# Kernel tuning notes

Measured on AMD Instinct MI355X. Metric: run time of the kernel, lower is better.

Reference implementation:

```python
import jax, jax.numpy as jnp
import numpy as np

B, LQ, LM, D, H = 2, 2048, 2048, 1024, 16
DH = D // H  # 64

def setup_inputs() -> dict:
    key = jax.random.key(0)
    ks = jax.random.split(key, 11)
    s = 0.02
    return {
        "query": jax.random.normal(ks[0], (B, LQ, D), jnp.float32),
        "memory": jax.random.normal(ks[1], (B, LM, D), jnp.float32),
        "memory_bias": jax.random.normal(ks[2], (B, LM), jnp.float32),
        "Wq": jax.random.normal(ks[3], (D, D), jnp.float32) * s,
        "bq": jnp.zeros((D,), jnp.float32),
        "Wk": jax.random.normal(ks[4], (D, D), jnp.float32) * s,
        "bk": jnp.zeros((D,), jnp.float32),
        "Wv": jax.random.normal(ks[5], (D, D), jnp.float32) * s,
        "bv": jnp.zeros((D,), jnp.float32),
        "Wo": jax.random.normal(ks[6], (D, D), jnp.float32) * s,
        "bo": jnp.zeros((D,), jnp.float32),
    }

def reference(query, memory, memory_bias, Wq, bq, Wk, bk, Wv, bv, Wo, bo):
    # QKV projections, split into heads: [B, L, H, DH]
    q = (query @ Wq + bq).reshape(B, LQ, H, DH)
    k = (memory @ Wk + bk).reshape(B, LM, H, DH)
    v = (memory @ Wv + bv).reshape(B, LM, H, DH)
    q = q * (DH ** -0.5)
    # logits: [B, H, Lq, Lk] (matches torch.einsum('btnh,bfnh->bnft', k, q))
    logits = jnp.einsum("bfnh,btnh->bnft", q, k)
    logits = logits + memory_bias[:, None, None, :]  # bias [B, Lm] -> [B,1,1,Lk]
    weights = jax.nn.softmax(logits, axis=-1)
    # dropout omitted (eval / rate 0 for correctness baseline)
    attn = jnp.einsum("bnft,btnh->bfnh", weights, v).reshape(B, LQ, D)
    return attn @ Wo + bo  # [B, Lq, output_depth]
```

## Files before the change

kernel.cpp:

```cpp
#include <hip/hip_runtime.h>
#include <hip/hip_bf16.h>
#include <math.h>


typedef __bf16 bf16;
typedef __bf16 bf16x4 __attribute__((ext_vector_type(4)));
typedef __bf16 bf16x8 __attribute__((ext_vector_type(8)));
typedef float f32x4 __attribute__((ext_vector_type(4)));

#define MFMA16(a, b, c) __builtin_amdgcn_mfma_f32_16x16x32_bf16((a), (b), (c), 0, 0, 0)

__device__ inline float exp2_hw(float x) {
    float r; asm("v_exp_f32 %0, %1" : "=v"(r) : "v"(x)); return r;
}

__device__ inline void gload_lds16(const bf16* g, bf16* l) {
    __builtin_amdgcn_global_load_lds(
        (const __attribute__((address_space(1))) void*)g,
        (__attribute__((address_space(3))) void*)l, 16, 0, 0);
}

__global__ __launch_bounds__(256) void prep_kernel(
    const float* __restrict__ query, const float* __restrict__ memory,
    const float* __restrict__ mbias,
    const float* __restrict__ W0, const float* __restrict__ W1,
    const float* __restrict__ W2, const float* __restrict__ W3,
    bf16* __restrict__ Yq, bf16* __restrict__ Ym, float* __restrict__ sbias,
    bf16* __restrict__ T0, bf16* __restrict__ T1,
    bf16* __restrict__ T2, bf16* __restrict__ T3)
{
    __shared__ float Ls[64][65];
    const int t = threadIdx.x;

    if (blockIdx.z == 0) {
        const float* X = blockIdx.y ? memory : query;
        bf16* Y = blockIdx.y ? Ym : Yq;
        const size_t i = ((size_t)blockIdx.x * 256 + t) * 8;
        float4 f0 = *(const float4*)&X[i];
        float4 f1 = *(const float4*)&X[i + 4];
        bf16x8 h;
        h[0] = (bf16)f0.x; h[1] = (bf16)f0.y; h[2] = (bf16)f0.z; h[3] = (bf16)f0.w;
        h[4] = (bf16)f1.x; h[5] = (bf16)f1.y; h[6] = (bf16)f1.z; h[7] = (bf16)f1.w;
        *(bf16x8*)&Y[i] = h;
        return;
    }
    const int x = blockIdx.x;
    if (x == 1024) {
        const int i = blockIdx.y * 2048 + t * 8;
        #pragma unroll
        for (int j = 0; j < 8; ++j) sbias[i + j] = mbias[i + j] * 1.44269504f;
        return;
    }
    if (x > 1024 || blockIdx.y) return;

    const int wsel = x >> 8, sub = x & 255;
    const float* W; bf16* T;
    switch (wsel) {
        case 0:  W = W0; T = T0; break;
        case 1:  W = W1; T = T1; break;
        case 2:  W = W2; T = T2; break;
        default: W = W3; T = T3; break;
    }
    const int n0 = (sub & 15) * 64, k0 = (sub >> 4) * 64;
    const int g = t >> 4, c = (t & 15) * 4;
    #pragma unroll
    for (int p = 0; p < 4; ++p) {
        const int row = p * 16 + g;
        float4 f = *(const float4*)&W[(size_t)(k0 + row) * 1024 + n0 + c];
        Ls[row][c + 0] = f.x; Ls[row][c + 1] = f.y;
        Ls[row][c + 2] = f.z; Ls[row][c + 3] = f.w;
    }
    __syncthreads();
    #pragma unroll
    for (int p = 0; p < 4; ++p) {
        const int n = p * 16 + g;
        bf16x4 h;
        h[0] = (bf16)Ls[c + 0][n]; h[1] = (bf16)Ls[c + 1][n];
        h[2] = (bf16)Ls[c + 2][n]; h[3] = (bf16)Ls[c + 3][n];
        *(bf16x4*)&T[(size_t)(n0 + n) * 1024 + k0 + c] = h;
    }
}

template <typename TO>
__global__ __launch_bounds__(256) void gemm_kernel(
    const bf16* __restrict__ A, const bf16* __restrict__ WT,
    const float* __restrict__ bias, TO* __restrict__ out,
    float alpha, int mode)
{
    __shared__ __align__(16) bf16 As[2][128 * 64];
    __shared__ __align__(16) bf16 Bs[2][64 * 64];

    const int fid = blockIdx.x + (blockIdx.y << 4);
    const int swz = (fid & 7) * 64 + (fid >> 3);
    const int n0 = (swz & 15) * 64;
    const int m0 = (swz >> 4) * 128;

    const int tid = threadIdx.x;
    const int w = tid >> 6, lane = tid & 63;
    const int lr = lane & 15, lg = lane >> 4;
    const int wm = (w >> 1) * 64, wn = (w & 1) * 32;

    const int arow0 = w * 32 + (lane >> 3);
    const int brow0 = w * 16 + (lane >> 3);
    const int sch = lane & 7;

    f32x4 acc[4][2] = {};

    auto stageG = [&](int kt, int bi) {
        #pragma unroll
        for (int p = 0; p < 4; ++p) {
            const int row = arow0 + p * 8;
            const int xc = ((sch ^ (row & 7)) << 3);
            gload_lds16(&A[(size_t)(m0 + row) * 1024 + kt + xc],
                        &As[bi][row * 64 + sch * 8]);
        }
        #pragma unroll
        for (int p = 0; p < 2; ++p) {
            const int row = brow0 + p * 8;
            const int xc = ((sch ^ (row & 7)) << 3);
            gload_lds16(&WT[(size_t)(n0 + row) * 1024 + kt + xc],
                        &Bs[bi][row * 64 + sch * 8]);
        }
    };

    stageG(0, 0);
    __syncthreads();

    int cur = 0;
    #pragma unroll 1
    for (int t = 0; t < 16; ++t) {
        if (t < 15) stageG((t + 1) * 64, cur ^ 1);

        #pragma unroll
        for (int ks = 0; ks < 2; ++ks) {
            const int c = (((ks * 4 + lg) ^ (lr & 7)) << 3);
            bf16x8 af[4], bfv[2];
            #pragma unroll
            for (int mt = 0; mt < 4; ++mt)
                af[mt] = *(const bf16x8*)&As[cur][(wm + mt * 16 + lr) * 64 + c];
            #pragma unroll
            for (int nt = 0; nt < 2; ++nt)
                bfv[nt] = *(const bf16x8*)&Bs[cur][(wn + nt * 16 + lr) * 64 + c];
            #pragma unroll
            for (int nt = 0; nt < 2; ++nt)
                #pragma unroll
                for (int mt = 0; mt < 4; ++mt)
                    acc[mt][nt] = MFMA16(af[mt], bfv[nt], acc[mt][nt]);
        }
        __syncthreads();
        cur ^= 1;
    }

    #pragma unroll
    for (int nt = 0; nt < 2; ++nt) {
        const int n = n0 + wn + nt * 16 + lr;
        const float bv = bias[n];
        #pragma unroll
        for (int mt = 0; mt < 4; ++mt) {
            #pragma unroll
            for (int i = 0; i < 4; ++i) {
                const int m = m0 + wm + mt * 16 + lg * 4 + i;
                const float v = (acc[mt][nt][i] + bv) * alpha;
                if (mode == 0) {
                    out[(size_t)m * 1024 + n] = (TO)v;
                } else {
                    const int b = m >> 11, t2 = m & 2047;
                    out[((size_t)(b << 10) + n) * 2048 + t2] = (TO)v;
                }
            }
        }
    }
}

__global__ __launch_bounds__(256) void gemm_kv_kernel(
    const bf16* __restrict__ A, const bf16* __restrict__ WTk,
    const bf16* __restrict__ WTv, const float* __restrict__ bk,
    const float* __restrict__ bv, bf16* __restrict__ Kout,
    bf16* __restrict__ Vtout)
{
    __shared__ __align__(16) bf16 As[2][128 * 64];
    __shared__ __align__(16) bf16 Bk[2][64 * 64];
    __shared__ __align__(16) bf16 Bv[2][64 * 64];

    const int fid = blockIdx.x + (blockIdx.y << 4);
    const int swz = (fid & 7) * 64 + (fid >> 3);
    const int n0 = (swz & 15) * 64;
    const int m0 = (swz >> 4) * 128;

    const int tid = threadIdx.x;
    const int w = tid >> 6, lane = tid & 63;
    const int lr = lane & 15, lg = lane >> 4;
    const int wm = (w >> 1) * 64, wn = (w & 1) * 32;

    const int arow0 = w * 32 + (lane >> 3);
    const int brow0 = w * 16 + (lane >> 3);
    const int sch = lane & 7;

    f32x4 accK[4][2] = {}, accV[4][2] = {};

    auto stageG = [&](int kt, int bi) {
        #pragma unroll
        for (int p = 0; p < 4; ++p) {
            const int row = arow0 + p * 8;
            const int xc = ((sch ^ (row & 7)) << 3);
            gload_lds16(&A[(size_t)(m0 + row) * 1024 + kt + xc],
                        &As[bi][row * 64 + sch * 8]);
        }
        #pragma unroll
        for (int p = 0; p < 2; ++p) {
            const int row = brow0 + p * 8;
            const int xc = ((sch ^ (row & 7)) << 3);
            gload_lds16(&WTk[(size_t)(n0 + row) * 1024 + kt + xc],
                        &Bk[bi][row * 64 + sch * 8]);
            gload_lds16(&WTv[(size_t)(n0 + row) * 1024 + kt + xc],
                        &Bv[bi][row * 64 + sch * 8]);
        }
    };

    stageG(0, 0);
    __syncthreads();

    int cur = 0;
    #pragma unroll 1
    for (int t = 0; t < 16; ++t) {
        if (t < 15) stageG((t + 1) * 64, cur ^ 1);

        #pragma unroll
        for (int ks = 0; ks < 2; ++ks) {
            const int c = (((ks * 4 + lg) ^ (lr & 7)) << 3);
            bf16x8 af[4], bkf[2], bvf[2];
            #pragma unroll
            for (int mt = 0; mt < 4; ++mt)
                af[mt] = *(const bf16x8*)&As[cur][(wm + mt * 16 + lr) * 64 + c];
            #pragma unroll
            for (int nt = 0; nt < 2; ++nt) {
                bkf[nt] = *(const bf16x8*)&Bk[cur][(wn + nt * 16 + lr) * 64 + c];
                bvf[nt] = *(const bf16x8*)&Bv[cur][(wn + nt * 16 + lr) * 64 + c];
            }
            #pragma unroll
            for (int nt = 0; nt < 2; ++nt)
                #pragma unroll
                for (int mt = 0; mt < 4; ++mt) {
                    accK[mt][nt] = MFMA16(af[mt], bkf[nt], accK[mt][nt]);
                    accV[mt][nt] = MFMA16(af[mt], bvf[nt], accV[mt][nt]);
                }
        }
        __syncthreads();
        cur ^= 1;
    }

    #pragma unroll
    for (int nt = 0; nt < 2; ++nt) {
        const int n = n0 + wn + nt * 16 + lr;
        const float bkv = bk[n], bvv = bv[n];
        #pragma unroll
        for (int mt = 0; mt < 4; ++mt) {
            #pragma unroll
            for (int i = 0; i < 4; ++i) {
                const int m = m0 + wm + mt * 16 + lg * 4 + i;
                Kout[(size_t)m * 1024 + n] = (bf16)(accK[mt][nt][i] + bkv);
                const int b = m >> 11, t2 = m & 2047;
                Vtout[((size_t)(b << 10) + n) * 2048 + t2] = (bf16)(accV[mt][nt][i] + bvv);
            }
        }
    }
}

__global__ __launch_bounds__(512) void attn_kernel(
    const bf16* __restrict__ Q, const bf16* __restrict__ K,
    const bf16* __restrict__ Vt, const float* __restrict__ sbias,
    bf16* __restrict__ Oout)
{
    __shared__ __align__(16) bf16 Kbuf[4][4096];
    __shared__ __align__(16) bf16 Vbuf[4][4096];

    const int tid = threadIdx.x;
    const int w = tid >> 6, lane = tid & 63;
    const int lr = lane & 15, lg = lane >> 4;

    const int fid = blockIdx.x + (blockIdx.y << 3) + (blockIdx.z << 7);
    const int swz = (fid & 7) * 32 + (fid >> 3);
    const int qt = swz & 7, head = (swz >> 3) & 15, b = swz >> 7;
    const int qrow = qt * 256 + w * 32;

    bf16x8 qf[2][2];
    #pragma unroll
    for (int g = 0; g < 2; ++g) {
        const size_t qo = (size_t)(b * 2048 + qrow + g * 16 + lr) * 1024 + head * 64;
        qf[g][0] = *(const bf16x8*)&Q[qo + lg * 8];
        qf[g][1] = *(const bf16x8*)&Q[qo + 32 + lg * 8];
    }

    const bf16* Kb = K + (size_t)b * 2048 * 1024 + head * 64;
    const bf16* Vb = Vt + ((size_t)b * 1024 + head * 64) * 2048;
    const float* biasb = sbias + b * 2048;

    float m_run[2] = {-INFINITY, -INFINITY};
    f32x4 of[2][4] = {};
    f32x4 ofl[2] = {};

    bf16x8 ones8;
    #pragma unroll
    for (int j = 0; j < 8; ++j) ones8[j] = (bf16)1.0f;

    const int R = tid >> 3, cc = tid & 7;
    const int cs = cc ^ (R & 7);
    const int piR = ((R & 16) << 1) | ((R & 12) << 1) | ((R & 32) >> 3) | (R & 3);
    auto stage = [&](int t, int slot) {
        gload_lds16(Kb + (size_t)(t * 64 + piR) * 1024 + cs * 8,
                    &Kbuf[slot][tid * 8]);
        gload_lds16(Vb + (size_t)R * 2048 + t * 64 + cs * 8,
                    &Vbuf[slot][tid * 8]);
    };

    stage(0, 0);
    stage(1, 1);

    f32x4 b4[4];
    b4[0] = *(const f32x4*)&biasb[8 * lg];
    b4[1] = *(const f32x4*)&biasb[32 + 8 * lg];
    b4[2] = *(const f32x4*)&biasb[4 + 8 * lg];
    b4[3] = *(const f32x4*)&biasb[36 + 8 * lg];

    #pragma unroll 1
    for (int it = 0; it < 32; ++it) {
        const int slot = it & 3;
        const int tn = (it < 30) ? it + 2 : 31;
        stage(tn, (it + 2) & 3);
        asm volatile("s_waitcnt vmcnt(4)" ::: "memory");
        __builtin_amdgcn_s_barrier();
        __builtin_amdgcn_sched_barrier(0);

        const int bt = ((it < 31) ? it + 1 : 31) * 64;
        f32x4 b4n[4];
        b4n[0] = *(const f32x4*)&biasb[bt + 8 * lg];
        b4n[1] = *(const f32x4*)&biasb[bt + 32 + 8 * lg];
        b4n[2] = *(const f32x4*)&biasb[bt + 4 + 8 * lg];
        b4n[3] = *(const f32x4*)&biasb[bt + 36 + 8 * lg];

        f32x4 s[2][4];
        #pragma unroll
        for (int g = 0; g < 2; ++g)
            #pragma unroll
            for (int nt = 0; nt < 4; ++nt) s[g][nt] = b4[nt];
        #pragma unroll
        for (int ks = 0; ks < 2; ++ks) {
            const int cw = (((ks * 4 + lg) ^ (lr & 7)) << 3);
            bf16x8 kf[4];
            #pragma unroll
            for (int nt = 0; nt < 4; ++nt)
                kf[nt] = *(const bf16x8*)&Kbuf[slot][(nt * 16 + lr) * 64 + cw];
            __builtin_amdgcn_s_setprio(1);
            #pragma unroll
            for (int nt = 0; nt < 4; ++nt) {
                s[0][nt] = MFMA16(kf[nt], qf[0][ks], s[0][nt]);
                s[1][nt] = MFMA16(kf[nt], qf[1][ks], s[1][nt]);
            }
            __builtin_amdgcn_s_setprio(0);
        }

        bf16x8 vf[2][4];
        #pragma unroll
        for (int ks = 0; ks < 2; ++ks) {
            const int cw = (((ks * 4 + lg) ^ (lr & 7)) << 3);
            #pragma unroll
            for (int dt = 0; dt < 4; ++dt)
                vf[ks][dt] = *(const bf16x8*)&Vbuf[slot][(dt * 16 + lr) * 64 + cw];
        }

        float rml[2];
        #pragma unroll
        for (int g = 0; g < 2; ++g) {
            float m0 = fmaxf(fmaxf(s[g][0][0], s[g][0][1]), fmaxf(s[g][0][2], s[g][0][3]));
            float m1 = fmaxf(fmaxf(s[g][1][0], s[g][1][1]), fmaxf(s[g][1][2], s[g][1][3]));
            float m2 = fmaxf(fmaxf(s[g][2][0], s[g][2][1]), fmaxf(s[g][2][2], s[g][2][3]));
            float m3 = fmaxf(fmaxf(s[g][3][0], s[g][3][1]), fmaxf(s[g][3][2], s[g][3][3]));
            rml[g] = fmaxf(fmaxf(m0, m1), fmaxf(m2, m3));
        }
        const bool need = (rml[0] > m_run[0] + 8.f) || (rml[1] > m_run[1] + 8.f);

        if (__any(need)) {
            #pragma unroll
            for (int g = 0; g < 2; ++g) {
                float mx = fmaxf(rml[g], __shfl_xor(rml[g], 16, 64));
                mx = fmaxf(mx, __shfl_xor(mx, 32, 64));
                const float mnew = fmaxf(m_run[g], mx);
                const float al = exp2_hw(m_run[g] - mnew);
                m_run[g] = mnew;
                ofl[g] *= al;
                #pragma unroll
                for (int dt = 0; dt < 4; ++dt) of[g][dt] *= al;
            }
        }

        bf16x8 pb[2][2];
        #pragma unroll
        for (int g = 0; g < 2; ++g)
            #pragma unroll
            for (int i = 0; i < 4; ++i) {
                pb[g][0][i]     = (bf16)exp2_hw(s[g][0][i] - m_run[g]);
                pb[g][1][i]     = (bf16)exp2_hw(s[g][1][i] - m_run[g]);
                pb[g][0][4 + i] = (bf16)exp2_hw(s[g][2][i] - m_run[g]);
                pb[g][1][4 + i] = (bf16)exp2_hw(s[g][3][i] - m_run[g]);
            }

        __builtin_amdgcn_s_setprio(1);
        #pragma unroll
        for (int ks = 0; ks < 2; ++ks) {
            #pragma unroll
            for (int g = 0; g < 2; ++g) {
                #pragma unroll
                for (int dt = 0; dt < 4; ++dt)
                    of[g][dt] = MFMA16(vf[ks][dt], pb[g][ks], of[g][dt]);
                ofl[g] = MFMA16(ones8, pb[g][ks], ofl[g]);
            }
        }
        __builtin_amdgcn_s_setprio(0);

        #pragma unroll
        for (int nt = 0; nt < 4; ++nt) b4[nt] = b4n[nt];
    }

    #pragma unroll
    for (int g = 0; g < 2; ++g) {
        const float inv = 1.0f / ofl[g][0];
        const size_t ob = (size_t)(b * 2048 + qrow + g * 16 + lr) * 1024 + head * 64;
        #pragma unroll
        for (int dt = 0; dt < 4; ++dt) {
            bf16x4 h4;
            #pragma unroll
            for (int i = 0; i < 4; ++i) h4[i] = (bf16)(of[g][dt][i] * inv);
            *(bf16x4*)&Oout[ob + dt * 16 + lg * 4] = h4;
        }
    }
}

extern "C" void kernel_launch(void* const* d_in, const int* in_sizes, int n_in,
                              void* d_out, int out_size, void* d_ws, size_t ws_size,
                              hipStream_t stream) {
    const float* query  = (const float*)d_in[0];
    const float* memory = (const float*)d_in[1];
    const float* mbias  = (const float*)d_in[2];
    const float* Wq = (const float*)d_in[3];
    const float* bq = (const float*)d_in[4];
    const float* Wk = (const float*)d_in[5];
    const float* bk = (const float*)d_in[6];
    const float* Wv = (const float*)d_in[7];
    const float* bv = (const float*)d_in[8];
    const float* Wo = (const float*)d_in[9];
    const float* bo = (const float*)d_in[10];
    float* out = (float*)d_out;

    const size_t SZ = 4096ull * 1024ull * sizeof(bf16);
    const size_t WZ = 1024ull * 1024ull * sizeof(bf16);
    char* ws = (char*)d_ws;
    bf16* Qp  = (bf16*)(ws);
    bf16* Kp  = (bf16*)(ws + SZ);
    bf16* Vtp = (bf16*)(ws + 2 * SZ);
    bf16* Ap  = (bf16*)(ws + 3 * SZ);
    bf16* WTq = (bf16*)(ws + 4 * SZ);
    bf16* WTk = (bf16*)(ws + 4 * SZ + WZ);
    bf16* WTv = (bf16*)(ws + 4 * SZ + 2 * WZ);
    bf16* WTo = (bf16*)(ws + 4 * SZ + 3 * WZ);
    float* sbias = (float*)(ws + 4 * SZ + 4 * WZ);

    dim3 blk(256);
    prep_kernel<<<dim3(2048, 2, 2), blk, 0, stream>>>(
        query, memory, mbias, Wq, Wk, Wv, Wo, Kp, Ap, sbias, WTq, WTk, WTv, WTo);

    dim3 gg(16, 32);
    gemm_kernel<bf16><<<gg, blk, 0, stream>>>(Kp, WTq, bq, Qp, 0.18033688f, 0);
    gemm_kv_kernel<<<gg, blk, 0, stream>>>(Ap, WTk, WTv, bk, bv, Kp, Vtp);
    attn_kernel<<<dim3(8, 16, 2), dim3(512), 0, stream>>>(Qp, Kp, Vtp, sbias, Ap);
    gemm_kernel<float><<<gg, blk, 0, stream>>>(Ap, WTo, bo, out, 1.0f, 0);
}
```

Baseline: 120.7 us.

## Process two KV tiles per attention loop iteration with one sync point

Unrolls the flash-attention main loop to handle two 64-key tiles per iteration. Both QK^T MFMA blocks are issued up front, and the two softmax/PV phases follow. Two tiles are staged ahead into the four-slot LDS ring, with one wait and a start/end barrier pair per tile pair instead of one barrier per tile. Bias is now loaded per pair and added after the MFMA instead of seeding the accumulator. The aim is more independent MFMA work to hide softmax latency and fewer barriers, at the cost of higher VGPR pressure and possible occupancy loss.

```diff
diff --git a/kernel.cpp b/kernel.cpp
--- a/kernel.cpp
+++ b/kernel.cpp
@@ -316,70 +316,83 @@
     stage(0, 0);
     stage(1, 1);
 
-    f32x4 b4[4];
-    b4[0] = *(const f32x4*)&biasb[8 * lg];
-    b4[1] = *(const f32x4*)&biasb[32 + 8 * lg];
-    b4[2] = *(const f32x4*)&biasb[4 + 8 * lg];
-    b4[3] = *(const f32x4*)&biasb[36 + 8 * lg];
-
     #pragma unroll 1
-    for (int it = 0; it < 32; ++it) {
-        const int slot = it & 3;
-        const int tn = (it < 30) ? it + 2 : 31;
-        stage(tn, (it + 2) & 3);
-        asm volatile("s_waitcnt vmcnt(4)" ::: "memory");
+    for (int it = 0; it < 32; it += 2) {
+        const int sa = it & 3, sb = (it + 1) & 3;
+        stage(it + 2 < 32 ? it + 2 : 31, (it + 2) & 3);
+        stage(it + 3 < 32 ? it + 3 : 31, (it + 3) & 3);
+
+        const int bta = it * 64, btb = bta + 64;
+        f32x4 ba[4], bb[4];
+        ba[0] = *(const f32x4*)&biasb[bta + 8 * lg];
+        ba[1] = *(const f32x4*)&biasb[bta + 32 + 8 * lg];
+        ba[2] = *(const f32x4*)&biasb[bta + 4 + 8 * lg];
+        ba[3] = *(const f32x4*)&biasb[bta + 36 + 8 * lg];
+        bb[0] = *(const f32x4*)&biasb[btb + 8 * lg];
+        bb[1] = *(const f32x4*)&biasb[btb + 32 + 8 * lg];
+        bb[2] = *(const f32x4*)&biasb[btb + 4 + 8 * lg];
+        bb[3] = *(const f32x4*)&biasb[btb + 36 + 8 * lg];
+
+        asm volatile("s_waitcnt vmcnt(12)" ::: "memory");
         __builtin_amdgcn_s_barrier();
         __builtin_amdgcn_sched_barrier(0);
 
-        const int bt = ((it < 31) ? it + 1 : 31) * 64;
-        f32x4 b4n[4];
-        b4n[0] = *(const f32x4*)&biasb[bt + 8 * lg];
-        b4n[1] = *(const f32x4*)&biasb[bt + 32 + 8 * lg];
-        b4n[2] = *(const f32x4*)&biasb[bt + 4 + 8 * lg];
-        b4n[3] = *(const f32x4*)&biasb[bt + 36 + 8 * lg];
-
-        f32x4 s[2][4];
-        #pragma unroll
-        for (int g = 0; g < 2; ++g)
-            #pragma unroll
-            for (int nt = 0; nt < 4; ++nt) s[g][nt] = b4[nt];
+        f32x4 sA[2][4] = {}, sB[2][4] = {};
         #pragma unroll
         for (int ks = 0; ks < 2; ++ks) {
             const int cw = (((ks * 4 + lg) ^ (lr & 7)) << 3);
             bf16x8 kf[4];
             #pragma unroll
             for (int nt = 0; nt < 4; ++nt)
-                kf[nt] = *(const bf16x8*)&Kbuf[slot][(nt * 16 + lr) * 64 + cw];
+                kf[nt] = *(const bf16x8*)&Kbuf[sa][(nt * 16 + lr) * 64 + cw];
             __builtin_amdgcn_s_setprio(1);
             #pragma unroll
             for (int nt = 0; nt < 4; ++nt) {
-                s[0][nt] = MFMA16(kf[nt], qf[0][ks], s[0][nt]);
-                s[1][nt] = MFMA16(kf[nt], qf[1][ks], s[1][nt]);
+                sA[0][nt] = MFMA16(kf[nt], qf[0][ks], sA[0][nt]);
+                sA[1][nt] = MFMA16(kf[nt], qf[1][ks], sA[1][nt]);
             }
             __builtin_amdgcn_s_setprio(0);
         }
-
-        bf16x8 vf[2][4];
         #pragma unroll
         for (int ks = 0; ks < 2; ++ks) {
             const int cw = (((ks * 4 + lg) ^ (lr & 7)) << 3);
+            bf16x8 kf[4];
+            #pragma unroll
+            for (int nt = 0; nt < 4; ++nt)
+                kf[nt] = *(const bf16x8*)&Kbuf[sb][(nt * 16 + lr) * 64 + cw];
+            __builtin_amdgcn_s_setprio(1);
+            #pragma unroll
+            for (int nt = 0; nt < 4; ++nt) {
+                sB[0][nt] = MFMA16(kf[nt], qf[0][ks], sB[0][nt]);
+                sB[1][nt] = MFMA16(kf[nt], qf[1][ks], sB[1][nt]);
+            }
+            __builtin_amdgcn_s_setprio(0);
+        }
+
+        bf16x8 vfA[2][4];
+        #pragma unroll
+        for (int ks = 0; ks < 2; ++ks) {
+            const int cw = (((ks * 4 + lg) ^ (lr & 7)) << 3);
             #pragma unroll
             for (int dt = 0; dt < 4; ++dt)
-                vf[ks][dt] = *(const bf16x8*)&Vbuf[slot][(dt * 16 + lr) * 64 + cw];
-        }
+                vfA[ks][dt] = *(const bf16x8*)&Vbuf[sa][(dt * 16 + lr) * 64 + cw];
+        }
+
+        #pragma unroll
+        for (int g = 0; g < 2; ++g)
+            #pragma unroll
+            for (int nt = 0; nt < 4; ++nt) sA[g][nt] += ba[nt];
 
         float rml[2];
         #pragma unroll
         for (int g = 0; g < 2; ++g) {
-            float m0 = fmaxf(fmaxf(s[g][0][0], s[g][0][1]), fmaxf(s[g][0][2], s[g][0][3]));
-            float m1 = fmaxf(fmaxf(s[g][1][0], s[g][1][1]), fmaxf(s[g][1][2], s[g][1][3]));
-            float m2 = fmaxf(fmaxf(s[g][2][0], s[g][2][1]), fmaxf(s[g][2][2], s[g][2][3]));
-            float m3 = fmaxf(fmaxf(s[g][3][0], s[g][3][1]), fmaxf(s[g][3][2], s[g][3][3]));
+            float m0 = fmaxf(fmaxf(sA[g][0][0], sA[g][0][1]), fmaxf(sA[g][0][2], sA[g][0][3]));
+            float m1 = fmaxf(fmaxf(sA[g][1][0], sA[g][1][1]), fmaxf(sA[g][1][2], sA[g][1][3]));
+            float m2 = fmaxf(fmaxf(sA[g][2][0], sA[g][2][1]), fmaxf(sA[g][2][2], sA[g][2][3]));
+            float m3 = fmaxf(fmaxf(sA[g][3][0], sA[g][3][1]), fmaxf(sA[g][3][2], sA[g][3][3]));
             rml[g] = fmaxf(fmaxf(m0, m1), fmaxf(m2, m3));
         }
-        const bool need = (rml[0] > m_run[0] + 8.f) || (rml[1] > m_run[1] + 8.f);
-
-        if (__any(need)) {
+        if (__any((rml[0] > m_run[0] + 8.f) || (rml[1] > m_run[1] + 8.f))) {
             #pragma unroll
             for (int g = 0; g < 2; ++g) {
                 float mx = fmaxf(rml[g], __shfl_xor(rml[g], 16, 64));
@@ -392,33 +405,86 @@
                 for (int dt = 0; dt < 4; ++dt) of[g][dt] *= al;
             }
         }
-
-        bf16x8 pb[2][2];
+        bf16x8 pbA[2][2];
         #pragma unroll
         for (int g = 0; g < 2; ++g)
             #pragma unroll
             for (int i = 0; i < 4; ++i) {
-                pb[g][0][i]     = (bf16)exp2_hw(s[g][0][i] - m_run[g]);
-                pb[g][1][i]     = (bf16)exp2_hw(s[g][1][i] - m_run[g]);
-                pb[g][0][4 + i] = (bf16)exp2_hw(s[g][2][i] - m_run[g]);
-                pb[g][1][4 + i] = (bf16)exp2_hw(s[g][3][i] - m_run[g]);
-            }
-
+                pbA[g][0][i]     = (bf16)exp2_hw(sA[g][0][i] - m_run[g]);
+                pbA[g][1][i]     = (bf16)exp2_hw(sA[g][1][i] - m_run[g]);
+                pbA[g][0][4 + i] = (bf16)exp2_hw(sA[g][2][i] - m_run[g]);
+                pbA[g][1][4 + i] = (bf16)exp2_hw(sA[g][3][i] - m_run[g]);
+            }
         __builtin_amdgcn_s_setprio(1);
         #pragma unroll
-        for (int ks = 0; ks < 2; ++ks) {
+        for (int ks = 0; ks < 2; ++ks)
             #pragma unroll
             for (int g = 0; g < 2; ++g) {
                 #pragma unroll
                 for (int dt = 0; dt < 4; ++dt)
-                    of[g][dt] = MFMA16(vf[ks][dt], pb[g][ks], of[g][dt]);
-                ofl[g] = MFMA16(ones8, pb[g][ks], ofl[g]);
-            }
-        }
+                    of[g][dt] = MFMA16(vfA[ks][dt], pbA[g][ks], of[g][dt]);
+                ofl[g] = MFMA16(ones8, pbA[g][ks], ofl[g]);
+            }
         __builtin_amdgcn_s_setprio(0);
 
-        #pragma unroll
-        for (int nt = 0; nt < 4; ++nt) b4[nt] = b4n[nt];
+        bf16x8 vfB[2][4];
+        #pragma unroll
+        for (int ks = 0; ks < 2; ++ks) {
+            const int cw = (((ks * 4 + lg) ^ (lr & 7)) << 3);
+            #pragma unroll
+            for (int dt = 0; dt < 4; ++dt)
+                vfB[ks][dt] = *(const bf16x8*)&Vbuf[sb][(dt * 16 + lr) * 64 + cw];
+        }
+        #pragma unroll
+        for (int g = 0; g < 2; ++g)
+            #pragma unroll
+            for (int nt = 0; nt < 4; ++nt) sB[g][nt] += bb[nt];
+
+        #pragma unroll
+        for (int g = 0; g < 2; ++g) {
+            float m0 = fmaxf(fmaxf(sB[g][0][0], sB[g][0][1]), fmaxf(sB[g][0][2], sB[g][0][3]));
+            float m1 = fmaxf(fmaxf(sB[g][1][0], sB[g][1][1]), fmaxf(sB[g][1][2], sB[g][1][3]));
+            float m2 = fmaxf(fmaxf(sB[g][2][0], sB[g][2][1]), fmaxf(sB[g][2][2], sB[g][2][3]));
+            float m3 = fmaxf(fmaxf(sB[g][3][0], sB[g][3][1]), fmaxf(sB[g][3][2], sB[g][3][3]));
+            rml[g] = fmaxf(fmaxf(m0, m1), fmaxf(m2, m3));
+        }
+        if (__any((rml[0] > m_run[0] + 8.f) || (rml[1] > m_run[1] + 8.f))) {
+            #pragma unroll
+            for (int g = 0; g < 2; ++g) {
+                float mx = fmaxf(rml[g], __shfl_xor(rml[g], 16, 64));
+                mx = fmaxf(mx, __shfl_xor(mx, 32, 64));
+                const float mnew = fmaxf(m_run[g], mx);
+                const float al = exp2_hw(m_run[g] - mnew);
+                m_run[g] = mnew;
+                ofl[g] *= al;
+                #pragma unroll
+                for (int dt = 0; dt < 4; ++dt) of[g][dt] *= al;
+            }
+        }
+        bf16x8 pbB[2][2];
+        #pragma unroll
+        for (int g = 0; g < 2; ++g)
+            #pragma unroll
+            for (int i = 0; i < 4; ++i) {
+                pbB[g][0][i]     = (bf16)exp2_hw(sB[g][0][i] - m_run[g]);
+                pbB[g][1][i]     = (bf16)exp2_hw(sB[g][1][i] - m_run[g]);
+                pbB[g][0][4 + i] = (bf16)exp2_hw(sB[g][2][i] - m_run[g]);
+                pbB[g][1][4 + i] = (bf16)exp2_hw(sB[g][3][i] - m_run[g]);
+            }
+        __builtin_amdgcn_s_setprio(1);
+        #pragma unroll
+        for (int ks = 0; ks < 2; ++ks)
+            #pragma unroll
+            for (int g = 0; g < 2; ++g) {
+                #pragma unroll
+                for (int dt = 0; dt < 4; ++dt)
+                    of[g][dt] = MFMA16(vfB[ks][dt], pbB[g][ks], of[g][dt]);
+                ofl[g] = MFMA16(ones8, pbB[g][ks], ofl[g]);
+            }
+        __builtin_amdgcn_s_setprio(0);
+
+        __builtin_amdgcn_sched_barrier(0);
+        __builtin_amdgcn_s_barrier();
     }
 
     #pragma unroll
```

Result: slower. 129.2 us (+7.0%).
